# Kernel tuning notes

Measured on AMD Instinct MI355X. Metric: run time of the kernel, lower is better.

Reference implementation:

```python
import jax, jax.numpy as jnp
import numpy as np

H = 512      # hidden_size (hardcoded in prior split)
L = 3        # num_layers
NH = 8       # num_heads
B = 16384    # batch
LN_EPS = 1e-5


def layer_norm(x, g, b):
    m = x.mean(-1, keepdims=True)
    v = ((x - m) ** 2).mean(-1, keepdims=True)
    return (x - m) / jnp.sqrt(v + LN_EPS) * g + b


def cross_gen(src, tgt, ipw, ipb, qkv_w, qkv_b, ao_w, ao_b,
              ln1g, ln1b, ln2g, ln2b, f1w, f1b, f2w, f2b, opw, opb, rw):
    """CrossModalGenerator.forward(src, tgt) for the whole batch (seq_len == 1)."""
    bsz = src.shape[0]
    dh = H // NH
    x = src @ ipw.T + ipb  # input_proj
    for l in range(L):
        wq, wk, wv = jnp.split(qkv_w[l], 3, axis=0)
        bq, bk, bv = jnp.split(qkv_b[l], 3)
        q = (x @ wq.T + bq).reshape(bsz, NH, dh)
        k = (tgt @ wk.T + bk).reshape(bsz, NH, dh)
        v = (tgt @ wv.T + bv).reshape(bsz, NH, dh)
        # single key/value token -> softmax over 1 element == 1 (kept for faithful grads)
        scores = (q * k).sum(-1, keepdims=True) / jnp.sqrt(jnp.float32(dh))  # [B,NH,1]
        w = jax.nn.softmax(scores, axis=-1)
        attn = (w * v).reshape(bsz, H)
        attn = attn @ ao_w[l].T + ao_b[l]  # MHA out_proj
        x = layer_norm(x + attn, ln1g[l], ln1b[l])
        h = jax.nn.gelu(x @ f1w[l].T + f1b[l], approximate=False)
        h = h @ f2w[l].T + f2b[l]
        x = layer_norm(x + h, ln2g[l], ln2b[l])
    gen = x @ opw.T + opb  # output_proj
    return rw * tgt + (1.0 - rw) * gen


def setup_inputs() -> dict:
    key = jax.random.key(0)
    ks = iter(jax.random.split(key, 40))
    nk = lambda: next(ks)
    s = jnp.float32(0.02)  # weight scale for numerical sanity
    f32 = jnp.float32
    return {
        "image_features": jax.random.normal(nk(), (B, H), f32),
        "text_features": jax.random.normal(nk(), (B, H), f32),
        "g_ipw": jax.random.normal(nk(), (2, H, H), f32) * s,
        "g_ipb": jnp.zeros((2, H), f32),
        "g_qkv_w": jax.random.normal(nk(), (2, L, 3 * H, H), f32) * s,
        "g_qkv_b": jnp.zeros((2, L, 3 * H), f32),
        "g_ao_w": jax.random.normal(nk(), (2, L, H, H), f32) * s,
        "g_ao_b": jnp.zeros((2, L, H), f32),
        "g_ln1g": jnp.ones((2, L, H), f32),
        "g_ln1b": jnp.zeros((2, L, H), f32),
        "g_ln2g": jnp.ones((2, L, H), f32),
        "g_ln2b": jnp.zeros((2, L, H), f32),
        "g_f1w": jax.random.normal(nk(), (2, L, 4 * H, H), f32) * s,
        "g_f1b": jnp.zeros((2, L, 4 * H), f32),
        "g_f2w": jax.random.normal(nk(), (2, L, H, 4 * H), f32) * s,
        "g_f2b": jnp.zeros((2, L, H), f32),
        "g_opw": jax.random.normal(nk(), (2, H, H), f32) * s,
        "g_opb": jnp.zeros((2, H), f32),
        "g_rw": jnp.full((2,), 0.5, f32),  # residual_weight per generator
        "prior_w1": jax.random.normal(nk(), (2 * H, H), f32) * s,
        "prior_b1": jnp.zeros((2 * H,), f32),
        "prior_w2": jax.random.normal(nk(), (2 * H, 2 * H), f32) * s,
        "prior_b2": jnp.zeros((2 * H,), f32),
        "prior_emb": jax.random.normal(nk(), (1, H), f32),
        "missing_type": jax.random.randint(nk(), (B,), 0, 4, jnp.int32),
    }


def reference(image_features, text_features, g_ipw, g_ipb, g_qkv_w, g_qkv_b,
              g_ao_w, g_ao_b, g_ln1g, g_ln1b, g_ln2g, g_ln2b, g_f1w, g_f1b,
              g_f2w, g_f2b, g_opw, g_opb, g_rw, prior_w1, prior_b1, prior_w2,
              prior_b2, prior_emb, missing_type):
    def gen(i, src, tgt):
        return cross_gen(src, tgt, g_ipw[i], g_ipb[i], g_qkv_w[i], g_qkv_b[i],
                         g_ao_w[i], g_ao_b[i], g_ln1g[i], g_ln1b[i],
                         g_ln2g[i], g_ln2b[i], g_f1w[i], g_f1b[i],
                         g_f2w[i], g_f2b[i], g_opw[i], g_opb[i], g_rw[i])

    # MoE-style dense dispatch: run both generators on the full batch, select by type.
    gen_text = gen(0, image_features, text_features)  # img_to_text, missing_type==1
    gen_img = gen(1, text_features, image_features)   # text_to_img, missing_type==2

    prior = jax.nn.gelu(prior_emb @ prior_w1.T + prior_b1, approximate=False)
    prior = prior @ prior_w2.T + prior_b2  # [1, 2H]
    p_img, p_text = prior[:, :H], prior[:, H:]

    mt = missing_type[:, None]
    enhanced_img = jnp.where(mt == 2, gen_img, image_features)
    enhanced_img = jnp.where(mt == 3, p_img, enhanced_img)
    enhanced_text = jnp.where(mt == 1, gen_text, text_features)
    enhanced_text = jnp.where(mt == 3, p_text, enhanced_text)
    return enhanced_img, enhanced_text
```

## Files before the change

kernel.cpp:

```cpp
#include <hip/hip_runtime.h>
#include <hip/hip_bf16.h>
#include <math.h>

#define BDIM 16384
#define HDIM 512

typedef __bf16 bf16;
typedef float f32x4 __attribute__((ext_vector_type(4)));
typedef __bf16 bf16x8 __attribute__((ext_vector_type(8)));
typedef __bf16 bf16x4 __attribute__((ext_vector_type(4)));

#define WAITV(N) asm volatile("s_waitcnt vmcnt(" #N ")" ::: "memory")


__device__ __forceinline__ void gload16(const bf16* g, bf16* l) {
  __builtin_amdgcn_global_load_lds((const __attribute__((address_space(1))) void*)g,
                                   (__attribute__((address_space(3))) void*)l, 16, 0, 0);
}

__device__ __forceinline__ float gelu_exact(float x) {
  return 0.5f * x * (1.0f + erff(x * 0.70710678118654752f));
}
__device__ __forceinline__ float gelu_fast2(float x) {
  float x3 = x * x * x;
  float e = exp2f(fmaf(-0.1029432f, x3, -2.3022082f * x));
  return x * __builtin_amdgcn_rcpf(1.f + e);
}


__global__ void cvt_f32_bf16(const float* __restrict__ src, bf16* __restrict__ dst, int n4) {
  int i = blockIdx.x * blockDim.x + threadIdx.x;
  if (i >= n4) return;
  f32x4 v = *(const f32x4*)(src + (size_t)i * 4);
  bf16x4 o;
  o[0] = (bf16)v[0]; o[1] = (bf16)v[1]; o[2] = (bf16)v[2]; o[3] = (bf16)v[3];
  *(bf16x4*)(dst + (size_t)i * 4) = o;
}

__global__ void cvt_wvT(const float* __restrict__ qkv, bf16* __restrict__ dst) {
  __shared__ float t[32][33];
  int il = blockIdx.z;
  int bm = blockIdx.x * 32;
  int bk = blockIdx.y * 32;
  const float* s = qkv + (size_t)il * 786432 + 524288;
  int tx = threadIdx.x & 31, ty = threadIdx.x >> 5;
#pragma unroll
  for (int j = 0; j < 4; ++j)
    t[ty * 4 + j][tx] = s[(size_t)(bm + ty * 4 + j) * 512 + bk + tx];
  __syncthreads();
  bf16* d = dst + (size_t)il * 262144;
#pragma unroll
  for (int j = 0; j < 4; ++j)
    d[(size_t)(bk + ty * 4 + j) * 512 + bm + tx] = (bf16)t[tx][ty * 4 + j];
}

__global__ void zfill(float* __restrict__ p, int n) {
  int i = blockIdx.x * 256 + threadIdx.x;
  if (i < n) p[i] = 0.f;
}

__global__ void bias_combine(const float* __restrict__ aow, const float* __restrict__ qkvb,
                             const float* __restrict__ aob, float* __restrict__ bc) {
  int gid = blockIdx.x * 4 + (threadIdx.x >> 6);
  int il = gid >> 9;
  int lane = threadIdx.x & 63;
  const float* ar = aow + (size_t)gid * 512 + lane * 8;
  const float* bv = qkvb + il * 1536 + 1024 + lane * 8;
  float s = 0.f;
#pragma unroll
  for (int i = 0; i < 8; ++i) s += ar[i] * bv[i];
#pragma unroll
  for (int off = 32; off > 0; off >>= 1) s += __shfl_xor(s, off);
  if (lane == 0) bc[gid] = s + aob[gid];
}


template<int ACT, bool RES, int K>
__launch_bounds__(512, 1)
__global__ void gemm_t(const bf16* __restrict__ A, long long Az,
                       const bf16* __restrict__ W, long long Wz,
                       const float* __restrict__ bias, long long bz,
                       const bf16* X, long long Xz,
                       bf16* C, long long Cz, int ldc) {
  __shared__ bf16 lds[4][2][8192];
  const long long z = blockIdx.z;
  A += z * Az; W += z * Wz; bias += z * bz; C += z * Cz;
  if (RES) X += z * Xz;
  const int tid = threadIdx.x, lane = tid & 63, wid = tid >> 6;
  const int brow = blockIdx.x * 256, bcol = blockIdx.y * 256;
  const int wm = (wid >> 2) * 128;
  const int wn = (wid & 3) * 64;
  const int lr = lane & 15, kg = lane >> 4;
  const int ko = (kg ^ ((lr >> 1) & 3)) << 3;

  f32x4 acc[8][4] = {};

  const int sco = (((tid & 3) ^ ((tid >> 3) & 3)) << 3);
  const bf16* Ag = A + (size_t)(brow + (tid >> 2)) * K + sco;
  const bf16* Wg = W + (size_t)(bcol + (tid >> 2)) * K + sco;
  auto STAGE = [&](int s, int kt) {
#pragma unroll
    for (int h = 0; h < 2; ++h) {
      gload16(Ag + (size_t)h * 128 * K + kt * 32, &lds[s][0][h * 4096 + wid * 512]);
      gload16(Wg + (size_t)h * 128 * K + kt * 32, &lds[s][1][h * 4096 + wid * 512]);
    }
  };

  const int nt = K / 32;
  STAGE(0, 0); STAGE(1, 1); STAGE(2, 2);

  int slot = 0;
  for (int t = 0; t < nt; ++t) {
    if (t + 3 < nt) { STAGE((slot + 3) & 3, t + 3); WAITV(12); }
    else if (t + 2 < nt) WAITV(8);
    else if (t + 1 < nt) WAITV(4);
    else WAITV(0);
    __builtin_amdgcn_s_barrier();
    const bf16* LA = &lds[slot][0][0];
    const bf16* LB = &lds[slot][1][0];
    bf16x8 a[8], b[4];
#pragma unroll
    for (int n = 0; n < 4; ++n) b[n] = *(const bf16x8*)(LB + ((wn + n * 16 + lr) << 5) + ko);
#pragma unroll
    for (int m = 0; m < 8; ++m) a[m] = *(const bf16x8*)(LA + ((wm + m * 16 + lr) << 5) + ko);
    __builtin_amdgcn_s_setprio(1);
#pragma unroll
    for (int m = 0; m < 8; ++m)
#pragma unroll
      for (int n = 0; n < 4; ++n)
        acc[m][n] = __builtin_amdgcn_mfma_f32_16x16x32_bf16(b[n], a[m], acc[m][n], 0, 0, 0);
    __builtin_amdgcn_s_setprio(0);
    asm volatile("" ::: "memory");
    __builtin_amdgcn_s_barrier();
    slot = (slot + 1) & 3;
  }

  f32x4 bv4[4];
#pragma unroll
  for (int n = 0; n < 4; ++n)
    bv4[n] = *(const f32x4*)(bias + bcol + wn + n * 16 + kg * 4);
#pragma unroll
  for (int m = 0; m < 8; ++m) {
    int row = brow + wm + m * 16 + lr;
#pragma unroll
    for (int n = 0; n < 4; ++n) {
      int col = bcol + wn + n * 16 + kg * 4;
      f32x4 v;
#pragma unroll
      for (int j = 0; j < 4; ++j) {
        float t = acc[m][n][j] + bv4[n][j];
        if (ACT == 1) t = gelu_fast2(t);
        v[j] = t;
      }
      if (RES) {
        bf16x4 xv = *(const bf16x4*)(X + (size_t)row * 512 + col);
#pragma unroll
        for (int j = 0; j < 4; ++j) v[j] += (float)xv[j];
      }
      bf16x4 o;
#pragma unroll
      for (int j = 0; j < 4; ++j) o[j] = (bf16)v[j];
      *(bf16x4*)(C + (size_t)row * ldc + col) = o;
    }
  }
}


template<int MODE>
__global__ void ln_chain(const bf16* __restrict__ Y, const bf16* __restrict__ R,
                         const float* __restrict__ gA, const float* __restrict__ bA,
                         const float* __restrict__ gB, const float* __restrict__ bB,
                         bf16* __restrict__ O) {
  int lane = threadIdx.x & 63;
  int row = blockIdx.x * 4 + (threadIdx.x >> 6);
  int gen = row >> 14;
  size_t base = (size_t)row * HDIM + lane * 8;
  bf16x8 yv = *(const bf16x8*)(Y + base);
  float v[8], s = 0.f, q = 0.f;
#pragma unroll
  for (int i = 0; i < 8; ++i) { v[i] = (float)yv[i]; s += v[i]; q += v[i] * v[i]; }
#pragma unroll
  for (int off = 32; off > 0; off >>= 1) { s += __shfl_xor(s, off); q += __shfl_xor(q, off); }
  float mean = s * (1.f / HDIM);
  float rstd = rsqrtf(q * (1.f / HDIM) - mean * mean + 1e-5f);
  const float* gAp = gA + gen * 1536 + lane * 8;
  const float* bAp = bA + gen * 1536 + lane * 8;
  if (MODE == 0) {
    bf16x8 o;
#pragma unroll
    for (int i = 0; i < 8; ++i) o[i] = (bf16)((v[i] - mean) * rstd * gAp[i] + bAp[i]);
    *(bf16x8*)(O + base) = o;
    return;
  }
  bf16x8 rv = *(const bf16x8*)(R + base);
  float u[8]; s = 0.f; q = 0.f;
#pragma unroll
  for (int i = 0; i < 8; ++i) {
    u[i] = (v[i] - mean) * rstd * gAp[i] + bAp[i] + (float)rv[i];
    s += u[i]; q += u[i] * u[i];
  }
#pragma unroll
  for (int off = 32; off > 0; off >>= 1) { s += __shfl_xor(s, off); q += __shfl_xor(q, off); }
  float m2 = s * (1.f / HDIM);
  float r2 = rsqrtf(q * (1.f / HDIM) - m2 * m2 + 1e-5f);
  const float* gBp = gB + gen * 1536 + lane * 8;
  const float* bBp = bB + gen * 1536 + lane * 8;
  bf16x8 o;
#pragma unroll
  for (int i = 0; i < 8; ++i) o[i] = (bf16)((u[i] - m2) * r2 * gBp[i] + bBp[i]);
  *(bf16x8*)(O + base) = o;
}


__launch_bounds__(256)
__global__ void gemm128(const bf16* __restrict__ A, long long Az, int lda,
                        const bf16* __restrict__ W, long long Wz,
                        const float* __restrict__ bias, long long bz,
                        bf16* __restrict__ C, long long Cz, int ldc, int K) {
  __shared__ bf16 As[128 * 64];
  __shared__ bf16 Bs[128 * 64];
  const long long z = blockIdx.z;
  A += z * Az; W += z * Wz; bias += z * bz; C += z * Cz;
  const int tid = threadIdx.x;
  const int lane = tid & 63;
  const int wid = tid >> 6;
  const int brow = blockIdx.x * 128;
  const int bcol = blockIdx.y * 128;
  const int wr = (wid >> 1) * 64;
  const int wc = (wid & 1) * 64;
  const int lr = lane & 15;
  const int kg = lane >> 4;
  f32x4 acc[4][4] = {};
  const bf16* Abase = A + (size_t)(brow + (tid >> 3)) * lda + ((tid & 7) << 3);
  const bf16* Wbase = W + (size_t)(bcol + (tid >> 3)) * K + ((tid & 7) << 3);
  bf16* AsDst = As + wid * 512;
  bf16* BsDst = Bs + wid * 512;
  for (int k0 = 0; k0 < K; k0 += 64) {
#pragma unroll
    for (int j = 0; j < 4; ++j) {
      gload16(Abase + (size_t)j * 32 * lda + k0, AsDst + j * 2048);
      gload16(Wbase + (size_t)j * 32 * K + k0, BsDst + j * 2048);
    }
    __syncthreads();
#pragma unroll
    for (int kk = 0; kk < 64; kk += 32) {
      bf16x8 a[4], bq[4];
#pragma unroll
      for (int m = 0; m < 4; ++m)
        a[m] = *(const bf16x8*)(As + (wr + m * 16 + lr) * 64 + kk + kg * 8);
#pragma unroll
      for (int n = 0; n < 4; ++n)
        bq[n] = *(const bf16x8*)(Bs + (wc + n * 16 + lr) * 64 + kk + kg * 8);
#pragma unroll
      for (int m = 0; m < 4; ++m)
#pragma unroll
        for (int n = 0; n < 4; ++n)
          acc[m][n] = __builtin_amdgcn_mfma_f32_16x16x32_bf16(a[m], bq[n], acc[m][n], 0, 0, 0);
    }
    __syncthreads();
  }
  float bv[4];
#pragma unroll
  for (int n = 0; n < 4; ++n) bv[n] = bias[bcol + wc + n * 16 + lr];
#pragma unroll
  for (int m = 0; m < 4; ++m) {
    int row = brow + wr + m * 16 + kg * 4;
#pragma unroll
    for (int n = 0; n < 4; ++n) {
      int col = bcol + wc + n * 16 + lr;
#pragma unroll
      for (int j = 0; j < 4; ++j)
        C[(size_t)(row + j) * ldc + col] = (bf16)(acc[m][n][j] + bv[n]);
    }
  }
}


__global__ void prior_fc1(const float* __restrict__ emb, const float* __restrict__ w1,
                          const float* __restrict__ b1, float* __restrict__ h) {
  int j = blockIdx.x * 4 + (threadIdx.x >> 6);
  int lane = threadIdx.x & 63;
  const float* wr = w1 + (size_t)j * 512 + lane * 8;
  const float* e = emb + lane * 8;
  float s = 0.f;
#pragma unroll
  for (int i = 0; i < 8; ++i) s += e[i] * wr[i];
#pragma unroll
  for (int off = 32; off > 0; off >>= 1) s += __shfl_xor(s, off);
  if (lane == 0) h[j] = gelu_exact(s + b1[j]);
}

__global__ void prior_fc2(const float* __restrict__ h, const float* __restrict__ w2,
                          const float* __restrict__ b2, float* __restrict__ p) {
  int j = blockIdx.x * 4 + (threadIdx.x >> 6);
  int lane = threadIdx.x & 63;
  const float* wr = w2 + (size_t)j * 1024 + lane * 16;
  const float* e = h + lane * 16;
  float s = 0.f;
#pragma unroll
  for (int i = 0; i < 16; ++i) s += e[i] * wr[i];
#pragma unroll
  for (int off = 32; off > 0; off >>= 1) s += __shfl_xor(s, off);
  if (lane == 0) p[j] = s + b2[j];
}


__global__ void combine(const float* __restrict__ img, const float* __restrict__ txt,
                        const bf16* __restrict__ gen_t, const bf16* __restrict__ gen_i,
                        const float* __restrict__ prior, const int* __restrict__ mt,
                        const float* __restrict__ rw, float* __restrict__ out) {
  int i4 = blockIdx.x * blockDim.x + threadIdx.x;
  if (i4 >= BDIM * 128) return;
  int bb = i4 >> 7;
  int c = (i4 & 127) << 2;
  size_t idx = (size_t)bb * HDIM + c;
  int m = mt[bb];
  f32x4 iv = *(const f32x4*)(img + idx);
  f32x4 tv = *(const f32x4*)(txt + idx);
  f32x4 oi = iv, ot = tv;
  if (m == 2) {
    float r = rw[1];
    bf16x4 gv = *(const bf16x4*)(gen_i + idx);
#pragma unroll
    for (int k = 0; k < 4; ++k) oi[k] = r * iv[k] + (1.f - r) * (float)gv[k];
  } else if (m == 3) {
    oi = *(const f32x4*)(prior + c);
  }
  if (m == 1) {
    float r = rw[0];
    bf16x4 gv = *(const bf16x4*)(gen_t + idx);
#pragma unroll
    for (int k = 0; k < 4; ++k) ot[k] = r * tv[k] + (1.f - r) * (float)gv[k];
  } else if (m == 3) {
    ot = *(const f32x4*)(prior + 512 + c);
  }
  *(f32x4*)(out + idx) = oi;
  *(f32x4*)(out + (size_t)BDIM * HDIM + idx) = ot;
}


extern "C" void kernel_launch(void* const* d_in, const int* in_sizes, int n_in,
                              void* d_out, int out_size, void* d_ws, size_t ws_size,
                              hipStream_t stream) {
  const float* img  = (const float*)d_in[0];
  const float* txt  = (const float*)d_in[1];
  const float* ipw  = (const float*)d_in[2];
  const float* ipb  = (const float*)d_in[3];
  const float* qkvw = (const float*)d_in[4];
  const float* qkvb = (const float*)d_in[5];
  const float* aow  = (const float*)d_in[6];
  const float* aob  = (const float*)d_in[7];
  const float* ln1g = (const float*)d_in[8];
  const float* ln1b = (const float*)d_in[9];
  const float* ln2g = (const float*)d_in[10];
  const float* ln2b = (const float*)d_in[11];
  const float* f1w  = (const float*)d_in[12];
  const float* f1b  = (const float*)d_in[13];
  const float* f2w  = (const float*)d_in[14];
  const float* f2b  = (const float*)d_in[15];
  const float* opw  = (const float*)d_in[16];
  const float* opb  = (const float*)d_in[17];
  const float* rw   = (const float*)d_in[18];
  const float* pw1  = (const float*)d_in[19];
  const float* pb1  = (const float*)d_in[20];
  const float* pw2  = (const float*)d_in[21];
  const float* pb2  = (const float*)d_in[22];
  const float* pemb = (const float*)d_in[23];
  const int*   mt   = (const int*)d_in[24];
  float* out = (float*)d_out;

  const size_t B = BDIM;
  char* ws = (char*)d_ws;
  size_t off = 0;
  auto alloc = [&](size_t bytes) -> char* {
    char* p = ws + off;
    off += (bytes + 255) & ~(size_t)255;
    return p;
  };
  bf16* src_bf = (bf16*)alloc(2 * B * 512 * 2);
  bf16* ipw_bf = (bf16*)alloc((size_t)2 * 262144 * 2);
  bf16* wvT_bf = (bf16*)alloc((size_t)6 * 262144 * 2);
  bf16* ao_bf  = (bf16*)alloc((size_t)6 * 262144 * 2);
  bf16* f1_bf  = (bf16*)alloc((size_t)6 * 1048576 * 2);
  bf16* f2_bf  = (bf16*)alloc((size_t)6 * 1048576 * 2);
  bf16* op_bf  = (bf16*)alloc((size_t)2 * 262144 * 2);
  bf16* Wc_bf  = (bf16*)alloc((size_t)6 * 262144 * 2);
  float* bc    = (float*)alloc(6 * 512 * 4);
  float* zeros = (float*)alloc(512 * 4);
  float* ph    = (float*)alloc(1024 * 4);
  float* pout  = (float*)alloc(1024 * 4);
  bf16* xn     = (bf16*)alloc(2 * B * 512 * 2);
  bf16* hreg   = (bf16*)alloc((size_t)B * 2048 * 2);
  bf16* h0     = (bf16*)d_out;
  const long long HZ = (long long)(hreg - h0);

  auto cvt = [&](const float* s, bf16* d, size_t n) {
    int n4 = (int)(n / 4);
    cvt_f32_bf16<<<(n4 + 255) / 256, 256, 0, stream>>>(s, d, n4);
  };
  cvt(img, src_bf, B * 512);
  cvt(txt, src_bf + B * 512, B * 512);
  cvt(ipw, ipw_bf, 2 * 262144);
  cvt(aow, ao_bf, 6 * 262144);
  cvt(f1w, f1_bf, 6 * 1048576);
  cvt(f2w, f2_bf, 6 * 1048576);
  cvt(opw, op_bf, 2 * 262144);
  cvt_wvT<<<dim3(16, 16, 6), 256, 0, stream>>>(qkvw, wvT_bf);
  zfill<<<2, 256, 0, stream>>>(zeros, 512);
  bias_combine<<<768, 256, 0, stream>>>(aow, qkvb, aob, bc);
  gemm128<<<dim3(4, 4, 6), 256, 0, stream>>>(ao_bf, 262144, 512, wvT_bf, 262144,
                                             zeros, 0, Wc_bf, 262144, 512, 512);
  prior_fc1<<<256, 256, 0, stream>>>(pemb, pw1, pb1, ph);
  prior_fc2<<<256, 256, 0, stream>>>(ph, pw2, pb2, pout);

  const long long BS = (long long)B * 512;

  auto attn = [&](int l) {
    gemm_t<0, false, 512><<<dim3(64, 2, 2), 512, 0, stream>>>(
        src_bf + BS, -BS, Wc_bf + (size_t)l * 262144, 786432,
        bc + l * 512, 1536, nullptr, 0, hreg, BS, 512);
  };

  attn(0);
  gemm_t<0, true, 512><<<dim3(64, 2, 2), 512, 0, stream>>>(
      src_bf, BS, ipw_bf, 262144, ipb, 512, hreg, BS, xn, BS, 512);
  ln_chain<0><<<2 * BDIM / 4, 256, 0, stream>>>(xn, nullptr, ln1g, ln1b,
                                                nullptr, nullptr, xn);

  for (int l = 0; l < 3; ++l) {
    gemm_t<1, false, 512><<<dim3(64, 8, 2), 512, 0, stream>>>(
        xn, BS, f1_bf + (size_t)l * 1048576, 3145728,
        f1b + l * 2048, 6144, nullptr, 0, h0, HZ, 2048);
    gemm_t<0, true, 2048><<<dim3(64, 2, 2), 512, 0, stream>>>(
        h0, HZ, f2_bf + (size_t)l * 1048576, 3145728,
        f2b + l * 512, 1536, xn, BS, xn, BS, 512);
    if (l < 2) {
      attn(l + 1);
      ln_chain<1><<<2 * BDIM / 4, 256, 0, stream>>>(
          xn, hreg, ln2g + l * 512, ln2b + l * 512,
          ln1g + (l + 1) * 512, ln1b + (l + 1) * 512, xn);
    } else {
      ln_chain<0><<<2 * BDIM / 4, 256, 0, stream>>>(
          xn, nullptr, ln2g + l * 512, ln2b + l * 512, nullptr, nullptr, xn);
    }
  }

  gemm_t<0, false, 512><<<dim3(64, 2, 2), 512, 0, stream>>>(
      xn, BS, op_bf, 262144, opb, 512, nullptr, 0, hreg, BS, 512);

  combine<<<(BDIM * 128 + 255) / 256, 256, 0, stream>>>(img, txt, hreg, hreg + BS,
                                                        pout, mt, rw, out);
}
```

Before: 869.3 us.

## Rewrite GEMM main loop as 8-phase ping-pong pipeline with split LDS stages

Replaces the 4-slot K=32 staging loop with an 8-phase schedule over K=64 tiles. Each phase issues one half-tile global-to-LDS load, runs half the MFMAs for the current k-slice, and prefetches the next B or A fragments from LDS. The aim is to interleave loads, LDS reads and MFMAs more finely, so fewer waves stall at the barrier between steps. It adds more barriers per tile, and clamped redundant loads at the tail.

```diff
diff --git a/kernel.cpp b/kernel.cpp
--- a/kernel.cpp
+++ b/kernel.cpp
@@ -77,12 +77,12 @@
 
 template<int ACT, bool RES, int K>
 __launch_bounds__(512, 1)
-__global__ void gemm_t(const bf16* __restrict__ A, long long Az,
-                       const bf16* __restrict__ W, long long Wz,
-                       const float* __restrict__ bias, long long bz,
-                       const bf16* X, long long Xz,
-                       bf16* C, long long Cz, int ldc) {
-  __shared__ bf16 lds[4][2][8192];
+__global__ void gemm_8p(const bf16* __restrict__ A, long long Az,
+                        const bf16* __restrict__ W, long long Wz,
+                        const float* __restrict__ bias, long long bz,
+                        const bf16* X, long long Xz,
+                        bf16* C, long long Cz, int ldc) {
+  __shared__ bf16 lds[65536];
   const long long z = blockIdx.z;
   A += z * Az; W += z * Wz; bias += z * bz; C += z * Cz;
   if (RES) X += z * Xz;
@@ -98,42 +98,70 @@
   const int sco = (((tid & 3) ^ ((tid >> 3) & 3)) << 3);
   const bf16* Ag = A + (size_t)(brow + (tid >> 2)) * K + sco;
   const bf16* Wg = W + (size_t)(bcol + (tid >> 2)) * K + sco;
-  auto STAGE = [&](int s, int kt) {
-#pragma unroll
-    for (int h = 0; h < 2; ++h) {
-      gload16(Ag + (size_t)h * 128 * K + kt * 32, &lds[s][0][h * 4096 + wid * 512]);
-      gload16(Wg + (size_t)h * 128 * K + kt * 32, &lds[s][1][h * 4096 + wid * 512]);
-    }
+  const int nt = K / 64;
+
+  auto STG = [&](const bf16* gbase, int kt, int kh, int dstE) {
+    int ck = kt < nt ? kt : nt - 1;
+    const bf16* s = gbase + (size_t)ck * 64 + (size_t)kh * 32;
+    gload16(s, lds + dstE + wid * 512);
+    gload16(s + (size_t)128 * K, lds + dstE + 4096 + wid * 512);
   };
 
-  const int nt = K / 32;
-  STAGE(0, 0); STAGE(1, 1); STAGE(2, 2);
-
-  int slot = 0;
-  for (int t = 0; t < nt; ++t) {
-    if (t + 3 < nt) { STAGE((slot + 3) & 3, t + 3); WAITV(12); }
-    else if (t + 2 < nt) WAITV(8);
-    else if (t + 1 < nt) WAITV(4);
-    else WAITV(0);
-    __builtin_amdgcn_s_barrier();
-    const bf16* LA = &lds[slot][0][0];
-    const bf16* LB = &lds[slot][1][0];
-    bf16x8 a[8], b[4];
-#pragma unroll
-    for (int n = 0; n < 4; ++n) b[n] = *(const bf16x8*)(LB + ((wn + n * 16 + lr) << 5) + ko);
-#pragma unroll
-    for (int m = 0; m < 8; ++m) a[m] = *(const bf16x8*)(LA + ((wm + m * 16 + lr) << 5) + ko);
-    __builtin_amdgcn_s_setprio(1);
-#pragma unroll
-    for (int m = 0; m < 8; ++m)
-#pragma unroll
-      for (int n = 0; n < 4; ++n)
-        acc[m][n] = __builtin_amdgcn_mfma_f32_16x16x32_bf16(b[n], a[m], acc[m][n], 0, 0, 0);
-    __builtin_amdgcn_s_setprio(0);
-    asm volatile("" ::: "memory");
-    __builtin_amdgcn_s_barrier();
-    slot = (slot + 1) & 3;
-  }
+  STG(Ag, 0, 0, 0);          STG(Wg, 0, 0, 16384);
+  STG(Ag, 0, 1, 8192);       STG(Wg, 0, 1, 24576);
+  STG(Ag, 1, 0, 32768);      STG(Wg, 1, 0, 32768 + 16384);
+
+  bf16x8 a[8], b01[2], b23[2];
+
+#define RD_A(BASE)                                                             \
+  { _Pragma("unroll") for (int m = 0; m < 8; ++m)                              \
+      a[m] = *(const bf16x8*)(lds + (BASE) + ((wm + m * 16 + lr) << 5) + ko); }
+#define RD_B01(BASE)                                                           \
+  { b01[0] = *(const bf16x8*)(lds + (BASE) + ((wn + lr) << 5) + ko);           \
+    b01[1] = *(const bf16x8*)(lds + (BASE) + ((wn + 16 + lr) << 5) + ko); }
+#define RD_B23(BASE)                                                           \
+  { b23[0] = *(const bf16x8*)(lds + (BASE) + ((wn + 32 + lr) << 5) + ko);      \
+    b23[1] = *(const bf16x8*)(lds + (BASE) + ((wn + 48 + lr) << 5) + ko); }
+#define MM(N0, BB)                                                             \
+  { __builtin_amdgcn_s_setprio(1);                                             \
+    _Pragma("unroll") for (int m = 0; m < 8; ++m) {                            \
+      acc[m][N0]     = __builtin_amdgcn_mfma_f32_16x16x32_bf16(BB[0], a[m], acc[m][N0], 0, 0, 0);     \
+      acc[m][N0 + 1] = __builtin_amdgcn_mfma_f32_16x16x32_bf16(BB[1], a[m], acc[m][N0 + 1], 0, 0, 0); } \
+    __builtin_amdgcn_s_setprio(0); }
+#define BARW                                                                   \
+  WAITV(6); __builtin_amdgcn_s_barrier(); asm volatile("" ::: "memory");
+#define ENDP                                                                   \
+  asm volatile("" ::: "memory"); __builtin_amdgcn_s_barrier();
+
+  BARW
+  RD_A(0) RD_B01(16384)
+
+  const int niter = nt / 2;
+  for (int i = 0; i < niter; ++i) {
+    const int t = 2 * i;
+    STG(Ag, t + 1, 1, 32768 + 8192);
+    BARW  MM(0, b01)  RD_B23(16384)                      ENDP
+    STG(Wg, t + 1, 1, 32768 + 24576);
+    BARW  MM(2, b23)  RD_A(8192) RD_B01(24576)           ENDP
+    STG(Ag, t + 2, 0, 0);
+    BARW  MM(0, b01)  RD_B23(24576)                      ENDP
+    STG(Wg, t + 2, 0, 16384);
+    BARW  MM(2, b23)  RD_A(32768) RD_B01(49152)          ENDP
+    STG(Ag, t + 2, 1, 8192);
+    BARW  MM(0, b01)  RD_B23(49152)                      ENDP
+    STG(Wg, t + 2, 1, 24576);
+    BARW  MM(2, b23)  RD_A(40960) RD_B01(57344)          ENDP
+    STG(Ag, t + 3, 0, 32768);
+    BARW  MM(0, b01)  RD_B23(57344)                      ENDP
+    STG(Wg, t + 3, 0, 32768 + 16384);
+    BARW  MM(2, b23)  RD_A(0) RD_B01(16384)              ENDP
+  }
+#undef RD_A
+#undef RD_B01
+#undef RD_B23
+#undef MM
+#undef BARW
+#undef ENDP
 
   f32x4 bv4[4];
 #pragma unroll
@@ -148,9 +176,9 @@
       f32x4 v;
 #pragma unroll
       for (int j = 0; j < 4; ++j) {
-        float t = acc[m][n][j] + bv4[n][j];
-        if (ACT == 1) t = gelu_fast2(t);
-        v[j] = t;
+        float t2 = acc[m][n][j] + bv4[n][j];
+        if (ACT == 1) t2 = gelu_fast2(t2);
+        v[j] = t2;
       }
       if (RES) {
         bf16x4 xv = *(const bf16x4*)(X + (size_t)row * 512 + col);
@@ -416,22 +444,22 @@
   const long long BS = (long long)B * 512;
 
   auto attn = [&](int l) {
-    gemm_t<0, false, 512><<<dim3(64, 2, 2), 512, 0, stream>>>(
+    gemm_8p<0, false, 512><<<dim3(64, 2, 2), 512, 0, stream>>>(
         src_bf + BS, -BS, Wc_bf + (size_t)l * 262144, 786432,
         bc + l * 512, 1536, nullptr, 0, hreg, BS, 512);
   };
 
   attn(0);
-  gemm_t<0, true, 512><<<dim3(64, 2, 2), 512, 0, stream>>>(
+  gemm_8p<0, true, 512><<<dim3(64, 2, 2), 512, 0, stream>>>(
       src_bf, BS, ipw_bf, 262144, ipb, 512, hreg, BS, xn, BS, 512);
   ln_chain<0><<<2 * BDIM / 4, 256, 0, stream>>>(xn, nullptr, ln1g, ln1b,
                                                 nullptr, nullptr, xn);
 
   for (int l = 0; l < 3; ++l) {
-    gemm_t<1, false, 512><<<dim3(64, 8, 2), 512, 0, stream>>>(
+    gemm_8p<1, false, 512><<<dim3(64, 8, 2), 512, 0, stream>>>(
         xn, BS, f1_bf + (size_t)l * 1048576, 3145728,
         f1b + l * 2048, 6144, nullptr, 0, h0, HZ, 2048);
-    gemm_t<0, true, 2048><<<dim3(64, 2, 2), 512, 0, stream>>>(
+    gemm_8p<0, true, 2048><<<dim3(64, 2, 2), 512, 0, stream>>>(
         h0, HZ, f2_bf + (size_t)l * 1048576, 3145728,
         f2b + l * 512, 1536, xn, BS, xn, BS, 512);
     if (l < 2) {
@@ -445,7 +473,7 @@
     }
   }
 
-  gemm_t<0, false, 512><<<dim3(64, 2, 2), 512, 0, stream>>>(
+  gemm_8p<0, false, 512><<<dim3(64, 2, 2), 512, 0, stream>>>(
       xn, BS, op_bf, 262144, opb, 512, nullptr, 0, hreg, BS, 512);
 
   combine<<<(BDIM * 128 + 255) / 256, 256, 0, stream>>>(img, txt, hreg, hreg + BS,
```

Result: faster. 830.9 us (-4.4%).
